# Kernel optimization log

Measured on AMD Instinct MI355X. Metric: run time of the kernel, lower is better.

The kernel has to match this reference:

```python
import jax, jax.numpy as jnp
import numpy as np

N, MA, F, NF = 512, 64, 128, 16
UPDATE_RATIO = 0.1
DECAY = 1.0
EPS = 1e-12  # avoids NaN grad of sqrt at self-distance 0 (torch diagonal is masked out by exp anyway)


def setup_inputs() -> dict:
    key = jax.random.key(0)
    ks = jax.random.split(key, 8)
    z = jax.random.randint(ks[0], (N, MA), 0, 10, dtype=jnp.int64) if jax.config.jax_enable_x64 else jax.random.randint(ks[0], (N, MA), 0, 10, dtype=jnp.int32)
    # pad last few atoms of each molecule with -1 to exercise the mask
    z = z.at[:, MA - 8:].set(-1)
    r = jax.random.normal(ks[1], (N, MA, 3), dtype=jnp.float32) * 3.0
    h = jax.random.normal(ks[2], (N, MA, F), dtype=jnp.float32)
    distances = jnp.linspace(0.5, 6.0, NF, dtype=jnp.float32)
    widths = jax.random.uniform(ks[3], (NF,), dtype=jnp.float32) * 0.5 + 0.5  # keep sigma > 0
    din = F * (1 + NF)  # 2176
    W1 = jax.random.normal(ks[4], (din, 512), dtype=jnp.float32) * (1.0 / np.sqrt(din))
    b1 = jnp.zeros((512,), dtype=jnp.float32)
    W2 = jax.random.normal(ks[5], (512, F), dtype=jnp.float32) * (1.0 / np.sqrt(512.0))
    b2 = jnp.zeros((F,), dtype=jnp.float32)
    return {"z": z, "r": r, "h": h, "distances": distances, "widths": widths,
            "W1": W1, "b1": b1, "W2": W2, "b2": b2}


def reference(z, r, h, distances, widths, W1, b1, W2, b2):
    n, ma = z.shape
    nf = distances.shape[0]
    # pairwise distance: (n, ma, ma)
    dv = r[:, :, None, :] - r[:, None, :, :]
    d = jnp.sqrt(jnp.sum(dv * dv, axis=-1) + EPS)
    mu = distances.reshape(1, nf, 1, 1)
    sigma = widths.reshape(1, nf, 1, 1)
    mask1 = (z > -1).astype(h.dtype)                      # (n, ma)
    pair_mask = mask1[:, :, None] * mask1[:, None, :]     # (n, ma, ma)
    # Gaussian RBF scores, masked: (n, nf, ma, ma)
    w = pair_mask[:, None] * jnp.exp(-((d[:, None] - mu) ** 2) / sigma) * 5.0
    # aggregate neighbor features: (n, ma, nf, F) -> (n, ma, nf*F)
    u = jnp.einsum('nfab,nbc->nafc', w, h).reshape(n, ma, nf * h.shape[-1])
    v = jnp.concatenate([h, u], axis=2)                   # (n, ma, F*(1+nf))
    v = jax.nn.silu(v @ W1 + b1) @ W2 + b2                # MLP 'net'
    h_new = h + v * UPDATE_RATIO * DECAY * mask1[:, :, None]
    return (z, r, h_new)
```

## Files before the change

### kernel.cpp

```cpp
#include <hip/hip_runtime.h>

#define MA 64
#define F 128
#define NF 16
#define HID 512
#define SLAB 8192
#define LDWB 144
#define LDT1B 1040
#define WL0 139264
#define WL1 148480
#define SWZ(row, col) ((((row) * 128) + (col)) ^ (((row) & 7) << 4))

typedef float  float4v __attribute__((ext_vector_type(4)));
typedef short  short8  __attribute__((ext_vector_type(8)));
typedef int    int8v   __attribute__((ext_vector_type(8)));

static __device__ __forceinline__ unsigned int pack2bf(float x, float y) {
    unsigned int a = __float_as_uint(x) + 0x8000u;
    unsigned int b = __float_as_uint(y) + 0x8000u;
    return __builtin_amdgcn_perm(b, a, 0x07060302u);
}
static __device__ __forceinline__ unsigned short f2bf1(float x) {
    return (unsigned short)((__float_as_uint(x) + 0x8000u) >> 16);
}
static __device__ __forceinline__ unsigned int pk4fp8(float a, float b, float c, float d) {
    int p = __builtin_amdgcn_cvt_pk_fp8_f32(a, b, 0, false);
    p = __builtin_amdgcn_cvt_pk_fp8_f32(c, d, p, true);
    return (unsigned int)p;
}

#define LGKM_BAR() do {                                        \
    asm volatile("s_waitcnt lgkmcnt(0)" ::: "memory");         \
    __builtin_amdgcn_s_barrier();                              \
    asm volatile("" ::: "memory");                             \
} while (0)

__global__ void pack_frags(const float* __restrict__ W1, const float* __restrict__ W2,
                           unsigned char* __restrict__ w1p, unsigned short* __restrict__ w2p) {
    int gid  = blockIdx.x * 4 + (threadIdx.x >> 6);
    int lane = threadIdx.x & 63;
    int arow = lane & 15;
    int kq   = lane >> 4;
    if (gid < 544) {
        int kt = gid >> 5, jt = gid & 31;
        const float* base = W1 + (size_t)(kt * 128 + kq * 32) * HID + jt * 16 + arow;
        unsigned int o[8];
        #pragma unroll
        for (int p = 0; p < 8; p++)
            o[p] = pk4fp8(base[(p * 4 + 0) * HID], base[(p * 4 + 1) * HID],
                          base[(p * 4 + 2) * HID], base[(p * 4 + 3) * HID]);
        unsigned char* dst = w1p + ((size_t)gid * 64 + lane) * 32;
        *(uint4*)dst        = (uint4){o[0], o[1], o[2], o[3]};
        *(uint4*)(dst + 16) = (uint4){o[4], o[5], o[6], o[7]};
    } else if (gid < 544 + 128) {
        int g2 = gid - 544;
        int kt = g2 >> 3, mt = g2 & 7;
        const float* base = W2 + (size_t)(kt * 32 + kq * 8) * F + mt * 16 + arow;
        short8 o;
        #pragma unroll
        for (int j = 0; j < 8; j++) o[j] = (short)f2bf1(base[j * F]);
        *(short8*)(w2p + ((size_t)g2 * 64 + lane) * 8) = o;
    }
}

__launch_bounds__(1024, 4)
__global__ void node_conv_mfma(const int* __restrict__ z, const float* __restrict__ rr,
        const float* __restrict__ h, const float* __restrict__ dist,
        const float* __restrict__ wid, const float* __restrict__ b1,
        const float* __restrict__ b2,
        const unsigned char* __restrict__ w1p, const unsigned short* __restrict__ w2p,
        float* __restrict__ out) {
    const int n = blockIdx.x;
    const int tid = threadIdx.x;
    const int lane = tid & 63;
    const int wave = tid >> 6;
    const int arow = lane & 15;
    const int quad = lane >> 4;
    const int kgrp = quad * 8;
    const int whi = wave >> 1;
    const int wlo = wave & 1;

    __shared__ __attribute__((aligned(16))) unsigned char lds[157696];
    __shared__ float r_lds[MA][5];

    const int N = gridDim.x;
    const float* hg = h + (size_t)n * MA * F;

    if (tid < MA) {
        int zi = z[n * MA + tid];
        out[(size_t)n * MA + tid] = (float)zi;
        r_lds[tid][0] = rr[(n * MA + tid) * 3 + 0];
        r_lds[tid][1] = rr[(n * MA + tid) * 3 + 1];
        r_lds[tid][2] = rr[(n * MA + tid) * 3 + 2];
        r_lds[tid][3] = (zi > -1) ? 1.0f : 0.0f;
    }
    if (tid < MA * 3)
        out[(size_t)N * MA + (size_t)n * MA * 3 + tid] = rr[(size_t)n * MA * 3 + tid];

    for (int i = tid; i < MA * F / 4; i += 1024) {
        float4 v = ((const float4*)hg)[i];
        int a = i >> 5, c4 = (i & 31) * 4;
        *(unsigned int*)&lds[SWZ(a, c4)] = pk4fp8(v.x, v.y, v.z, v.w);
    }
    short8 ah[2];
    {
        int c = whi * 16 + arow;
        #pragma unroll
        for (int ks2 = 0; ks2 < 2; ks2++)
            #pragma unroll
            for (int j = 0; j < 8; j++)
                ah[ks2][j] = (short)f2bf1(hg[(size_t)(ks2 * 32 + kgrp + j) * F + c]);
    }
    int8v p0, p1, q0, q1;
    {
        const unsigned char* pp = w1p + ((size_t)((wave * 2) * 64 + lane)) * 32;
        p0 = *(const int8v*)pp;
        p1 = *(const int8v*)(pp + 2048);
    }
    __syncthreads();

    const int wa = tid >> 4;
    const int wb0 = (tid & 15) * 4;
    float dpre[4];
    {
        float ax = r_lds[wa][0], ay = r_lds[wa][1], az = r_lds[wa][2];
        float am = r_lds[wa][3];
        #pragma unroll
        for (int j = 0; j < 4; j++) {
            float dx = ax - r_lds[wb0 + j][0];
            float dy = ay - r_lds[wb0 + j][1];
            float dz = az - r_lds[wb0 + j][2];
            float d = sqrtf(dx * dx + dy * dy + dz * dz + 1e-12f);
            float mm = am * r_lds[wb0 + j][3];
            dpre[j] = d + (1.0f - mm) * 1e4f;
        }
    }

    auto EXPW = [&](int fidx, int wlOff) {
        float mu = dist[fidx];
        float isg = 1.0f / wid[fidx];
        float e[4];
        #pragma unroll
        for (int j = 0; j < 4; j++) {
            float t = dpre[j] - mu;
            e[j] = 5.0f * __expf(-t * t * isg);
        }
        uint2 wp = { pack2bf(e[0], e[1]), pack2bf(e[2], e[3]) };
        *(uint2*)&lds[wlOff + wa * LDWB + wb0 * 2] = wp;
    };
    const float4v zf = {0.f, 0.f, 0.f, 0.f};
    auto UG = [&](int wlOff, int slabOff) {
        float4v ud0 = zf, ud1 = zf;
        #pragma unroll
        for (int ks2 = 0; ks2 < 2; ks2++) {
            short8 bw0 = *(const short8*)&lds[wlOff + ((wlo * 2 + 0) * 16 + arow) * LDWB + (ks2 * 32 + kgrp) * 2];
            ud0 = __builtin_amdgcn_mfma_f32_16x16x32_bf16(ah[ks2], bw0, ud0, 0, 0, 0);
            short8 bw1 = *(const short8*)&lds[wlOff + ((wlo * 2 + 1) * 16 + arow) * LDWB + (ks2 * 32 + kgrp) * 2];
            ud1 = __builtin_amdgcn_mfma_f32_16x16x32_bf16(ah[ks2], bw1, ud1, 0, 0, 0);
        }
        unsigned int u0 = pk4fp8(ud0[0], ud0[1], ud0[2], ud0[3]);
        unsigned int u1 = pk4fp8(ud1[0], ud1[1], ud1[2], ud1[3]);
        *(unsigned int*)&lds[slabOff + SWZ((wlo * 2 + 0) * 16 + arow, whi * 16 + quad * 4)] = u0;
        *(unsigned int*)&lds[slabOff + SWZ((wlo * 2 + 1) * 16 + arow, whi * 16 + quad * 4)] = u1;
    };

    EXPW(0, WL0);
    LGKM_BAR();
    for (int f = 0; f < NF; f++) {
        const int wlR = (f & 1) ? WL1 : WL0;
        const int wlW = (f & 1) ? WL0 : WL1;
        UG(wlR, (f + 1) * SLAB);
        if (f < NF - 1) EXPW(f + 1, wlW);
        LGKM_BAR();
    }

    float4v acc[2][4];
    #pragma unroll
    for (int i = 0; i < 2; i++)
        #pragma unroll
        for (int jv = 0; jv < 4; jv++) acc[i][jv] = zf;

    for (int f = 0; f <= NF; f++) {
        if (f < NF) {
            const unsigned char* pq = w1p + ((size_t)(((f + 1) * 32 + wave * 2) * 64 + lane)) * 32;
            q0 = *(const int8v*)pq;
            q1 = *(const int8v*)(pq + 2048);
        }
        const int sb = f * SLAB;
        #pragma unroll
        for (int at = 0; at < 4; at++) {
            const int rowb = at * 16 + arow;
            uint4 lo = *(const uint4*)&lds[sb + SWZ(rowb, quad * 32)];
            uint4 hi = *(const uint4*)&lds[sb + SWZ(rowb, quad * 32 + 16)];
            int8v bfr;
            bfr[0] = (int)lo.x; bfr[1] = (int)lo.y; bfr[2] = (int)lo.z; bfr[3] = (int)lo.w;
            bfr[4] = (int)hi.x; bfr[5] = (int)hi.y; bfr[6] = (int)hi.z; bfr[7] = (int)hi.w;
            acc[0][at] = __builtin_amdgcn_mfma_scale_f32_16x16x128_f8f6f4(
                p0, bfr, acc[0][at], 0, 0, 0, 127, 0, 127);
            acc[1][at] = __builtin_amdgcn_mfma_scale_f32_16x16x128_f8f6f4(
                p1, bfr, acc[1][at], 0, 0, 0, 127, 0, 127);
        }
        p0 = q0;
        p1 = q1;
    }
    LGKM_BAR();

    float4 b1v[2];
    #pragma unroll
    for (int mt = 0; mt < 2; mt++)
        b1v[mt] = *(const float4*)&b1[wave * 32 + mt * 16 + quad * 4];

    #pragma unroll
    for (int mt = 0; mt < 2; mt++) {
        #pragma unroll
        for (int at = 0; at < 4; at++) {
            float xs[4];
            #pragma unroll
            for (int r = 0; r < 4; r++) {
                float x = acc[mt][at][r] + ((const float*)&b1v[mt])[r];
                xs[r] = x / (1.0f + __expf(-x));
            }
            uint2 pv = { pack2bf(xs[0], xs[1]), pack2bf(xs[2], xs[3]) };
            *(uint2*)&lds[(at * 16 + arow) * LDT1B + (wave * 32 + mt * 16 + quad * 4) * 2] = pv;
        }
    }
    LGKM_BAR();

    float4v g2[2] = { zf, zf };

    short8 awA = *(const short8*)(w2p + ((size_t)(whi) * 64 + lane) * 8);
    #pragma unroll
    for (int ks2 = 0; ks2 < 8; ks2++) {
        const int k1 = 2 * ks2 + 1;
        short8 awB = *(const short8*)(w2p + ((size_t)(k1 * 8 + whi) * 64 + lane) * 8);
        #pragma unroll
        for (int j = 0; j < 2; j++) {
            short8 bt = *(const short8*)&lds[((wlo * 2 + j) * 16 + arow) * LDT1B + ((2 * ks2) * 32 + kgrp) * 2];
            g2[j] = __builtin_amdgcn_mfma_f32_16x16x32_bf16(awA, bt, g2[j], 0, 0, 0);
        }
        const int k2 = (ks2 < 7) ? 2 * ks2 + 2 : 0;
        awA = *(const short8*)(w2p + ((size_t)(k2 * 8 + whi) * 64 + lane) * 8);
        #pragma unroll
        for (int j = 0; j < 2; j++) {
            short8 bt = *(const short8*)&lds[((wlo * 2 + j) * 16 + arow) * LDT1B + ((2 * ks2 + 1) * 32 + kgrp) * 2];
            g2[j] = __builtin_amdgcn_mfma_f32_16x16x32_bf16(awB, bt, g2[j], 0, 0, 0);
        }
    }

    float* outh = out + (size_t)N * MA * 4 + (size_t)n * MA * F;
    const int c0 = whi * 16 + quad * 4;
    float4 b2v = *(const float4*)&b2[c0];
    #pragma unroll
    for (int j = 0; j < 2; j++) {
        int a = (wlo * 2 + j) * 16 + arow;
        float m = r_lds[a][3] * 0.1f;
        float4 hv = *(const float4*)&hg[a * F + c0];
        float4 res;
        res.x = hv.x + (g2[j][0] + b2v.x) * m;
        res.y = hv.y + (g2[j][1] + b2v.y) * m;
        res.z = hv.z + (g2[j][2] + b2v.z) * m;
        res.w = hv.w + (g2[j][3] + b2v.w) * m;
        *(float4*)&outh[(size_t)a * F + c0] = res;
    }
}

extern "C" void kernel_launch(void* const* d_in, const int* in_sizes, int n_in,
                              void* d_out, int out_size, void* d_ws, size_t ws_size,
                              hipStream_t stream) {
    const int*   z    = (const int*)d_in[0];
    const float* rr   = (const float*)d_in[1];
    const float* h    = (const float*)d_in[2];
    const float* dist = (const float*)d_in[3];
    const float* wid  = (const float*)d_in[4];
    const float* W1   = (const float*)d_in[5];
    const float* b1   = (const float*)d_in[6];
    const float* W2   = (const float*)d_in[7];
    const float* b2   = (const float*)d_in[8];
    float* out = (float*)d_out;

    int Nmol = in_sizes[0] / MA;

    unsigned char*  w1p = (unsigned char*)d_ws;
    unsigned short* w2p = (unsigned short*)(w1p + (size_t)544 * 64 * 32);

    pack_frags<<<168, 256, 0, stream>>>(W1, W2, w1p, w2p);
    node_conv_mfma<<<Nmol, 1024, 0, stream>>>(z, rr, h, dist, wid, b1, b2, w1p, w2p, out);
}
```

Baseline: 150.1 us.

## Compute all RBF weights upfront and let each wave own one filter's aggregation

Replaces the 16-step filter loop, where all waves cooperated on one filter per step with a block barrier each time, with a single pass. Every filter's Gaussian weights are first written into the slabs, then each of the 16 waves runs the whole h^T·W product for its own filter and overwrites that filter's slab in place with fp8 results. h is transposed into a new bf16 LDS region instead of being held in registers, so the two weight ping-pong buffers are gone. This removes 16 barriers but raises per-wave register pressure and adds an in-place slab overwrite that relies on each wave reading its weights before writing.

```diff
diff --git a/kernel.cpp b/kernel.cpp
--- a/kernel.cpp
+++ b/kernel.cpp
@@ -5,10 +5,8 @@
 #define NF 16
 #define HID 512
 #define SLAB 8192
-#define LDWB 144
+#define HT 139264
 #define LDT1B 1040
-#define WL0 139264
-#define WL1 148480
 #define SWZ(row, col) ((((row) * 128) + (col)) ^ (((row) & 7) << 4))
 
 typedef float  float4v __attribute__((ext_vector_type(4)));
@@ -80,7 +78,7 @@
     const int whi = wave >> 1;
     const int wlo = wave & 1;
 
-    __shared__ __attribute__((aligned(16))) unsigned char lds[157696];
+    __shared__ __attribute__((aligned(16))) unsigned char lds[155648];
     __shared__ float r_lds[MA][5];
 
     const int N = gridDim.x;
@@ -102,20 +100,9 @@
         int a = i >> 5, c4 = (i & 31) * 4;
         *(unsigned int*)&lds[SWZ(a, c4)] = pk4fp8(v.x, v.y, v.z, v.w);
     }
-    short8 ah[2];
-    {
-        int c = whi * 16 + arow;
-        #pragma unroll
-        for (int ks2 = 0; ks2 < 2; ks2++)
-            #pragma unroll
-            for (int j = 0; j < 8; j++)
-                ah[ks2][j] = (short)f2bf1(hg[(size_t)(ks2 * 32 + kgrp + j) * F + c]);
-    }
-    int8v p0, p1, q0, q1;
-    {
-        const unsigned char* pp = w1p + ((size_t)((wave * 2) * 64 + lane)) * 32;
-        p0 = *(const int8v*)pp;
-        p1 = *(const int8v*)(pp + 2048);
+    for (int i = tid; i < MA * F; i += 1024) {
+        int b = i >> 7, c = i & 127;
+        *(unsigned short*)&lds[HT + SWZ(c, b * 2)] = f2bf1(hg[i]);
     }
     __syncthreads();
 
@@ -136,9 +123,10 @@
         }
     }
 
-    auto EXPW = [&](int fidx, int wlOff) {
-        float mu = dist[fidx];
-        float isg = 1.0f / wid[fidx];
+    #pragma unroll
+    for (int f = 0; f < NF; f++) {
+        float mu = dist[f];
+        float isg = 1.0f / wid[f];
         float e[4];
         #pragma unroll
         for (int j = 0; j < 4; j++) {
@@ -146,33 +134,60 @@
             e[j] = 5.0f * __expf(-t * t * isg);
         }
         uint2 wp = { pack2bf(e[0], e[1]), pack2bf(e[2], e[3]) };
-        *(uint2*)&lds[wlOff + wa * LDWB + wb0 * 2] = wp;
-    };
+        *(uint2*)&lds[(f + 1) * SLAB + SWZ(wa, wb0 * 2)] = wp;
+    }
+    LGKM_BAR();
+
     const float4v zf = {0.f, 0.f, 0.f, 0.f};
-    auto UG = [&](int wlOff, int slabOff) {
-        float4v ud0 = zf, ud1 = zf;
-        #pragma unroll
-        for (int ks2 = 0; ks2 < 2; ks2++) {
-            short8 bw0 = *(const short8*)&lds[wlOff + ((wlo * 2 + 0) * 16 + arow) * LDWB + (ks2 * 32 + kgrp) * 2];
-            ud0 = __builtin_amdgcn_mfma_f32_16x16x32_bf16(ah[ks2], bw0, ud0, 0, 0, 0);
-            short8 bw1 = *(const short8*)&lds[wlOff + ((wlo * 2 + 1) * 16 + arow) * LDWB + (ks2 * 32 + kgrp) * 2];
-            ud1 = __builtin_amdgcn_mfma_f32_16x16x32_bf16(ah[ks2], bw1, ud1, 0, 0, 0);
-        }
-        unsigned int u0 = pk4fp8(ud0[0], ud0[1], ud0[2], ud0[3]);
-        unsigned int u1 = pk4fp8(ud1[0], ud1[1], ud1[2], ud1[3]);
-        *(unsigned int*)&lds[slabOff + SWZ((wlo * 2 + 0) * 16 + arow, whi * 16 + quad * 4)] = u0;
-        *(unsigned int*)&lds[slabOff + SWZ((wlo * 2 + 1) * 16 + arow, whi * 16 + quad * 4)] = u1;
-    };
-
-    EXPW(0, WL0);
+
+    {
+        const int ws = (wave + 1) * SLAB;
+        short8 wB[4][2];
+        #pragma unroll
+        for (int at = 0; at < 4; at++)
+            #pragma unroll
+            for (int ks = 0; ks < 2; ks++)
+                wB[at][ks] = *(const short8*)&lds[ws + SWZ(at * 16 + arow, (ks * 32 + kgrp) * 2)];
+
+        #pragma unroll
+        for (int cp = 0; cp < 4; cp++) {
+            short8 hA[2][2];
+            #pragma unroll
+            for (int cc = 0; cc < 2; cc++)
+                #pragma unroll
+                for (int ks = 0; ks < 2; ks++)
+                    hA[cc][ks] = *(const short8*)&lds[HT + SWZ((cp * 2 + cc) * 16 + arow, (ks * 32 + kgrp) * 2)];
+            float4v ud[2][4];
+            #pragma unroll
+            for (int cc = 0; cc < 2; cc++)
+                #pragma unroll
+                for (int at = 0; at < 4; at++) ud[cc][at] = zf;
+            #pragma unroll
+            for (int cc = 0; cc < 2; cc++)
+                #pragma unroll
+                for (int at = 0; at < 4; at++)
+                    #pragma unroll
+                    for (int ks = 0; ks < 2; ks++)
+                        ud[cc][at] = __builtin_amdgcn_mfma_f32_16x16x32_bf16(
+                            hA[cc][ks], wB[at][ks], ud[cc][at], 0, 0, 0);
+            #pragma unroll
+            for (int cc = 0; cc < 2; cc++)
+                #pragma unroll
+                for (int at = 0; at < 4; at++) {
+                    unsigned int up = pk4fp8(ud[cc][at][0], ud[cc][at][1],
+                                             ud[cc][at][2], ud[cc][at][3]);
+                    *(unsigned int*)&lds[ws + SWZ(at * 16 + arow, (cp * 2 + cc) * 16 + quad * 4)] = up;
+                }
+        }
+    }
+
+    int8v p0, p1, q0, q1;
+    {
+        const unsigned char* pp = w1p + ((size_t)((wave * 2) * 64 + lane)) * 32;
+        p0 = *(const int8v*)pp;
+        p1 = *(const int8v*)(pp + 2048);
+    }
     LGKM_BAR();
-    for (int f = 0; f < NF; f++) {
-        const int wlR = (f & 1) ? WL1 : WL0;
-        const int wlW = (f & 1) ? WL0 : WL1;
-        UG(wlR, (f + 1) * SLAB);
-        if (f < NF - 1) EXPW(f + 1, wlW);
-        LGKM_BAR();
-    }
 
     float4v acc[2][4];
     #pragma unroll
```

Result: faster. 147.1 us (-2.0%).
